# Optimization experiments

Measured on AMD Instinct MI355X. Metric: run time of the kernel, lower is better.

Reference implementation:

```python
import jax, jax.numpy as jnp
import numpy as np

C = 512
NUM_GROUPS = 32
EPS = 1e-6


def group_norm(x, gamma, beta):
    # x: [B, C, H, W]
    B, Cc, H, W = x.shape
    xg = x.reshape(B, NUM_GROUPS, Cc // NUM_GROUPS, H, W)
    mean = xg.mean(axis=(2, 3, 4), keepdims=True)
    var = xg.var(axis=(2, 3, 4), keepdims=True)
    xn = (xg - mean) / jnp.sqrt(var + EPS)
    xn = xn.reshape(B, Cc, H, W)
    return xn * gamma[None, :, None, None] + beta[None, :, None, None]


def conv1x1(x, w, b):
    # w: [out_c, in_c], x: [B, C, H, W]
    return jnp.einsum('oc,bchw->bohw', w, x) + b[None, :, None, None]


def setup_inputs() -> dict:
    key = jax.random.key(0)
    ks = jax.random.split(key, 6)
    B, H, W = 2, 64, 64
    x = jax.random.normal(ks[0], (B, C, H, W), dtype=jnp.float32)
    s = 1.0 / np.sqrt(C)
    wq = jax.random.normal(ks[1], (C, C), dtype=jnp.float32) * s
    wk = jax.random.normal(ks[2], (C, C), dtype=jnp.float32) * s
    wv = jax.random.normal(ks[3], (C, C), dtype=jnp.float32) * s
    wo = jax.random.normal(ks[4], (C, C), dtype=jnp.float32) * s
    bq = jnp.zeros((C,), jnp.float32)
    bk = jnp.zeros((C,), jnp.float32)
    bv = jnp.zeros((C,), jnp.float32)
    bo = jnp.zeros((C,), jnp.float32)
    gamma = jnp.ones((C,), jnp.float32)
    beta = jnp.zeros((C,), jnp.float32)
    return {"x": x, "gamma": gamma, "beta": beta, "wq": wq, "bq": bq,
            "wk": wk, "bk": bk, "wv": wv, "bv": bv, "wo": wo, "bo": bo}


def reference(x, gamma, beta, wq, bq, wk, bk, wv, bv, wo, bo):
    B, Cc, H, W = x.shape
    h = group_norm(x, gamma, beta)
    q = conv1x1(h, wq, bq).reshape(B, Cc, H * W)  # [B, C, N]
    k = conv1x1(h, wk, bk).reshape(B, Cc, H * W)
    v = conv1x1(h, wv, bv).reshape(B, Cc, H * W)
    scale = Cc ** (-0.5)
    # scores a[b,i,j] = sum_c q[b,c,i] * k[b,c,j]
    a = jnp.einsum('bci,bcj->bij', q, k) * scale
    a = jax.nn.softmax(a, axis=2)
    # out[b,c,i] = sum_j v[b,c,j] * a[b,i,j]  (matches bmm(v, a^T))
    o = jnp.einsum('bcj,bij->bci', v, a).reshape(B, Cc, H, W)
    o = conv1x1(o, wo, bo)
    return x + o
```

## Files before the change

kernel.cpp:

```cpp
#include <hip/hip_runtime.h>
#include <stdint.h>

#define NPIX 4096
#define CDIM 512

typedef _Float16 hv8 __attribute__((ext_vector_type(8)));
typedef float f32x4 __attribute__((ext_vector_type(4)));

__device__ __forceinline__ void lds_direct16(const _Float16* g, _Float16* l) {
    __builtin_amdgcn_global_load_lds(
        (const __attribute__((address_space(1))) void*)g,
        (__attribute__((address_space(3))) void*)l, 16, 0, 0);
}

__global__ void cvt_w(const float* __restrict__ s0, const float* __restrict__ s1,
                      const float* __restrict__ s2, const float* __restrict__ s3,
                      _Float16* __restrict__ d0, _Float16* __restrict__ d1,
                      _Float16* __restrict__ d2, _Float16* __restrict__ d3) {
    int i = blockIdx.x * 256 + threadIdx.x;
    d0[i] = (_Float16)s0[i];
    d1[i] = (_Float16)s1[i];
    d2[i] = (_Float16)s2[i];
    d3[i] = (_Float16)s3[i];
}

__global__ void stats_kernel(const float* __restrict__ x, float* __restrict__ stats) {
    int idx = blockIdx.x;
    const float4* base = (const float4*)(x + (long)idx * 16 * NPIX);
    int tid = threadIdx.x;
    float s = 0.f, sq = 0.f;
    for (int it = 0; it < 64; ++it) {
        float4 f = base[it * 256 + tid];
        s  += f.x + f.y + f.z + f.w;
        sq += f.x * f.x + f.y * f.y + f.z * f.z + f.w * f.w;
    }
    __shared__ float rs[256], rq[256];
    rs[tid] = s; rq[tid] = sq;
    __syncthreads();
    for (int st = 128; st > 0; st >>= 1) {
        if (tid < st) { rs[tid] += rs[tid + st]; rq[tid] += rq[tid + st]; }
        __syncthreads();
    }
    if (tid == 0) {
        float mean = rs[0] * (1.0f / 65536.0f);
        float var  = rq[0] * (1.0f / 65536.0f) - mean * mean;
        stats[idx * 2]     = mean;
        stats[idx * 2 + 1] = rsqrtf(var + 1e-6f);
    }
}

__global__ void normT_kernel(const float* __restrict__ x, const float* __restrict__ stats,
                             const float* __restrict__ gamma, const float* __restrict__ beta,
                             _Float16* __restrict__ hT) {
    int b = blockIdx.z, c0 = blockIdx.x * 32, n0 = blockIdx.y * 32;
    int tid = threadIdx.x;
    __shared__ float t[32][33];
    int cl = tid >> 5;
    int nl = tid & 31;
    for (int r = 0; r < 4; ++r)
        t[r * 8 + cl][nl] = x[(long)b * CDIM * NPIX + (long)(c0 + r * 8 + cl) * NPIX + n0 + nl];
    __syncthreads();
    for (int r = 0; r < 4; ++r) {
        int nr = r * 8 + cl;
        int c = c0 + nl;
        float m    = stats[(b * 32 + (c >> 4)) * 2];
        float rstd = stats[(b * 32 + (c >> 4)) * 2 + 1];
        float val = (t[nl][nr] - m) * rstd * gamma[c] + beta[c];
        hT[(long)b * NPIX * CDIM + (long)(n0 + nr) * CDIM + c] = (_Float16)val;
    }
}

template<int EPI>
__launch_bounds__(256, 2)
__global__ void gemm_bt_kernel(const _Float16* __restrict__ A, const _Float16* __restrict__ BT,
                               void* __restrict__ D, const float* __restrict__ bias,
                               const float* __restrict__ resid,
                               int M, int N, int K,
                               long aBatch, long bBatch, long dBatch, long rBatch) {
    const int b = blockIdx.z;
    A  += (long)b * aBatch;
    BT += (long)b * bBatch;
    const int m0 = blockIdx.y * 128;
    const int n0 = blockIdx.x * 128;
    const int tid = threadIdx.x;
    const int l = tid & 63;
    const int w = tid >> 6;
    const int wm = (w >> 1) * 64;
    const int wn = (w & 1) * 64;
    const int lr = l & 15;
    const int lk = l >> 4;
    __shared__ __align__(16) _Float16 As[128 * 32];
    __shared__ __align__(16) _Float16 Bs[128 * 32];
    f32x4 acc[4][4] = {};
    const int nK = K >> 5;
    for (int kt = 0; kt < nK; ++kt) {
        const int kb = kt * 32;
#pragma unroll
        for (int c = 0; c < 2; ++c) {
            int chunk = c * 256 + tid;
            int row = chunk >> 2;
            int k8 = (chunk & 3) * 8;
            _Float16* ldsA = As + (size_t)(c * 256 + (tid & ~63)) * 8;
            _Float16* ldsB = Bs + (size_t)(c * 256 + (tid & ~63)) * 8;
            lds_direct16(A  + (long)(m0 + row) * K + kb + k8, ldsA);
            lds_direct16(BT + (long)(n0 + row) * K + kb + k8, ldsB);
        }
        __syncthreads();
        hv8 af[4], bfr[4];
#pragma unroll
        for (int mi = 0; mi < 4; ++mi)
            af[mi] = *(const hv8*)(As + (size_t)(wm + mi * 16 + lr) * 32 + lk * 8);
#pragma unroll
        for (int ni = 0; ni < 4; ++ni)
            bfr[ni] = *(const hv8*)(Bs + (size_t)(wn + ni * 16 + lr) * 32 + lk * 8);
#pragma unroll
        for (int mi = 0; mi < 4; ++mi)
#pragma unroll
            for (int ni = 0; ni < 4; ++ni)
                acc[mi][ni] = __builtin_amdgcn_mfma_f32_16x16x32_f16(af[mi], bfr[ni], acc[mi][ni], 0, 0, 0);
        __syncthreads();
    }
#pragma unroll
    for (int mi = 0; mi < 4; ++mi)
#pragma unroll
        for (int ni = 0; ni < 4; ++ni)
#pragma unroll
            for (int r = 0; r < 4; ++r) {
                int row = m0 + wm + mi * 16 + lk * 4 + r;
                int col = n0 + wn + ni * 16 + lr;
                float val = acc[mi][ni][r];
                if (EPI == 0) {
                    ((_Float16*)D)[(long)b * dBatch + (long)row * N + col] = (_Float16)(val + bias[col]);
                } else if (EPI == 1) {
                    ((_Float16*)D)[(long)b * dBatch + (long)row * N + col] = (_Float16)(val + bias[row]);
                } else {
                    long idx = (long)row * N + col;
                    ((float*)D)[(long)b * dBatch + idx] =
                        val + bias[row] + resid[(long)b * rBatch + idx];
                }
            }
}

__launch_bounds__(512, 2)
__global__ void attn_kernel(const _Float16* __restrict__ qT, const _Float16* __restrict__ kT,
                            const _Float16* __restrict__ v,
                            _Float16* __restrict__ p0, _Float16* __restrict__ p1,
                            float* __restrict__ lbuf) {
    __shared__ __align__(16) _Float16 Ks[2][32 * 512];
    __shared__ __align__(16) char ps[2][64 * 80];
    __shared__ float red[8][64];
    __shared__ float redt[64];

    const int g = blockIdx.x;
    const int xcd = g & 7;
    const int comb = xcd >> 1;
    const int itile = ((g >> 3) << 1) | (xcd & 1);
    const int batch = comb >> 1;
    const int jhalf = comb & 1;
    const int i0 = itile * 64;
    const int jbase = jhalf * 2048;

    const int tid = threadIdx.x;
    const int l = tid & 63, w = tid >> 6;
    const int lr = l & 15, lk = l >> 4;
    const int iq = w >> 1, jq = w & 1;

    const _Float16* qb = qT + (long)batch * NPIX * CDIM;
    const _Float16* kb = kT + (long)batch * NPIX * CDIM;
    const _Float16* vb = v  + (long)batch * CDIM * NPIX;

    hv8 af[16];
    {
        const _Float16* qr = qb + (long)(i0 + iq * 16 + lr) * CDIM + lk * 8;
#pragma unroll
        for (int kk = 0; kk < 16; ++kk)
            af[kk] = *(const hv8*)(qr + kk * 32);
    }

    f32x4 oacc[4][4] = {};
    float lsum[4] = {};
    hv8 vf[4];

    const _Float16* vptr = vb + (long)(w * 64 + lr) * NPIX + jbase + lk * 8;
    const float scale = 0.044194173824159216f;

#define STAGE(BUF, JT)                                                               \
    {                                                                                \
        const long j0s = (long)jbase + (JT) * 32;                                    \
        _Float16* kd = Ks[BUF];                                                      \
        _Pragma("unroll")                                                            \
        for (int q = 0; q < 4; ++q) {                                                \
            int row = q * 8 + w;                                                     \
            int cc = l ^ (row & 7);                                                  \
            lds_direct16(kb + (j0s + row) * CDIM + cc * 8, kd + row * 512);          \
        }                                                                            \
    }

#define VLOAD(JT)                                                                    \
    {                                                                                \
        _Pragma("unroll")                                                            \
        for (int ni = 0; ni < 4; ++ni)                                               \
            vf[ni] = *(const hv8*)(vptr + (long)ni * (16 * NPIX) + (JT) * 32);       \
    }

#define QKEXP(CUR)                                                                   \
    {                                                                                \
        const char* kbase = (const char*)Ks[CUR];                                    \
        f32x4 sa = {}, sb = {};                                                      \
        const int jj = jq * 16 + lr;                                                 \
        const uint32_t sw = (uint32_t)((jj & 7) << 4);                               \
        _Pragma("unroll")                                                            \
        for (int kk = 0; kk < 8; ++kk) {                                             \
            hv8 b0 = *(const hv8*)(kbase + (((uint32_t)(jj * 1024 + (2 * kk) * 64 + lk * 16)) ^ sw));     \
            sa = __builtin_amdgcn_mfma_f32_16x16x32_f16(af[2 * kk], b0, sa, 0, 0, 0);                     \
            hv8 b1 = *(const hv8*)(kbase + (((uint32_t)(jj * 1024 + (2 * kk + 1) * 64 + lk * 16)) ^ sw)); \
            sb = __builtin_amdgcn_mfma_f32_16x16x32_f16(af[2 * kk + 1], b1, sb, 0, 0, 0);                 \
        }                                                                            \
        sa += sb;                                                                    \
        _Pragma("unroll")                                                            \
        for (int r = 0; r < 4; ++r) {                                                \
            float p = __expf(sa[r] * scale);                                         \
            lsum[r] += p;                                                            \
            int i = iq * 16 + lk * 4 + r;                                            \
            int j2 = jq * 16 + lr;                                                   \
            *(_Float16*)(ps[CUR] + i * 80 + j2 * 2) = (_Float16)p;                   \
        }                                                                            \
    }

#define PVSTEP(PRV)                                                                  \
    {                                                                                \
        _Pragma("unroll")                                                            \
        for (int mi = 0; mi < 4; ++mi) {                                             \
            int i2 = mi * 16 + lr;                                                   \
            hv8 pa = *(const hv8*)(ps[PRV] + i2 * 80 + lk * 16);                     \
            _Pragma("unroll")                                                        \
            for (int ni = 0; ni < 4; ++ni)                                           \
                oacc[mi][ni] = __builtin_amdgcn_mfma_f32_16x16x32_f16(pa, vf[ni], oacc[mi][ni], 0, 0, 0); \
        }                                                                            \
    }

#define ENDBAR(N)                                                                    \
    __builtin_amdgcn_sched_barrier(0);                                               \
    asm volatile("s_waitcnt vmcnt(" #N ") lgkmcnt(0)" ::: "memory");                 \
    __builtin_amdgcn_s_barrier();                                                    \
    __builtin_amdgcn_sched_barrier(0);

#define STEP(JT, CUR)                                                                \
    {                                                                                \
        if ((JT) < 63) STAGE((CUR) ^ 1, (JT) + 1)                                    \
        __builtin_amdgcn_sched_barrier(0);                                           \
        __builtin_amdgcn_s_setprio(1);                                               \
        QKEXP(CUR)                                                                   \
        PVSTEP((CUR) ^ 1)                                                            \
        __builtin_amdgcn_s_setprio(0);                                               \
        __builtin_amdgcn_sched_barrier(0);                                           \
        VLOAD(JT)                                                                    \
        ENDBAR(4)                                                                    \
    }

    STAGE(0, 0)
    __builtin_amdgcn_sched_barrier(0);
    asm volatile("s_waitcnt vmcnt(0)" ::: "memory");
    __builtin_amdgcn_s_barrier();
    __builtin_amdgcn_sched_barrier(0);

    STAGE(1, 1)
    __builtin_amdgcn_s_setprio(1);
    QKEXP(0)
    __builtin_amdgcn_s_setprio(0);
    VLOAD(0)
    ENDBAR(4)

    for (int jt = 1; jt < 63; jt += 2) {
        STEP(jt,     1)
        STEP(jt + 1, 0)
    }
    STEP(63, 1)

    asm volatile("s_waitcnt vmcnt(0)" ::: "memory");
    __builtin_amdgcn_sched_barrier(0);
    PVSTEP(1)

#pragma unroll
    for (int m = 1; m <= 8; m <<= 1)
#pragma unroll
        for (int r = 0; r < 4; ++r)
            lsum[r] += __shfl_xor(lsum[r], m, 64);
    if (lr == 0)
#pragma unroll
        for (int r = 0; r < 4; ++r)
            red[w][iq * 16 + lk * 4 + r] = lsum[r];
    __syncthreads();
    if (tid < 64) {
        int iq2 = tid >> 4;
        float lv = red[iq2 * 2][tid] + red[iq2 * 2 + 1][tid];
        redt[tid] = 1.0f / lv;
        lbuf[jhalf * 8192 + batch * NPIX + i0 + tid] = lv;
    }
    __syncthreads();

    _Float16* dsth = (jhalf ? p1 : p0) + (long)batch * NPIX * CDIM;
#pragma unroll
    for (int mi = 0; mi < 4; ++mi)
#pragma unroll
        for (int r = 0; r < 4; ++r) {
            int row = mi * 16 + lk * 4 + r;
            float rv = redt[row];
#pragma unroll
            for (int ni = 0; ni < 4; ++ni) {
                int c = w * 64 + ni * 16 + lr;
                dsth[(long)(i0 + row) * CDIM + c] = (_Float16)(oacc[mi][ni][r] * rv);
            }
        }
#undef STEP
#undef ENDBAR
#undef PVSTEP
#undef QKEXP
#undef VLOAD
#undef STAGE
}

__global__ void combine_kernel(const _Float16* __restrict__ p0, const _Float16* __restrict__ p1,
                               const float* __restrict__ lbuf, _Float16* __restrict__ out) {
    long g = (long)blockIdx.x * 256 + threadIdx.x;
    long base = g * 8;
    int rowg = (int)(g >> 6);
    float l0 = lbuf[rowg], l1 = lbuf[8192 + rowg];
    float w0 = l0 / (l0 + l1);
    float w1 = 1.0f - w0;
    hv8 a = *(const hv8*)(p0 + base);
    hv8 b = *(const hv8*)(p1 + base);
    hv8 o;
#pragma unroll
    for (int i = 0; i < 8; ++i)
        o[i] = (_Float16)((float)a[i] * w0 + (float)b[i] * w1);
    *(hv8*)(out + base) = o;
}

extern "C" void kernel_launch(void* const* d_in, const int* in_sizes, int n_in,
                              void* d_out, int out_size, void* d_ws, size_t ws_size,
                              hipStream_t stream) {
    const float* x     = (const float*)d_in[0];
    const float* gamma = (const float*)d_in[1];
    const float* beta  = (const float*)d_in[2];
    const float* wq    = (const float*)d_in[3];
    const float* bq    = (const float*)d_in[4];
    const float* wk    = (const float*)d_in[5];
    const float* bk    = (const float*)d_in[6];
    const float* wv    = (const float*)d_in[7];
    const float* bv    = (const float*)d_in[8];
    const float* wo    = (const float*)d_in[9];
    const float* bo    = (const float*)d_in[10];
    float* out = (float*)d_out;

    char* ws = (char*)d_ws;
    float* stats = (float*)ws;
    _Float16* wqb = (_Float16*)(ws + 1024);
    _Float16* wkb = wqb + 262144;
    _Float16* wvb = wkb + 262144;
    _Float16* wob = wvb + 262144;
    _Float16* hT  = wob + 262144;
    const long TSZ = (long)2 * NPIX * CDIM;
    _Float16* qT = hT + TSZ;
    _Float16* kT = qT + TSZ;
    _Float16* vv = kT + TSZ;
    _Float16* oT = vv + TSZ;
    float* lbuf = (float*)(oT + TSZ);

    cvt_w<<<dim3(1024), dim3(256), 0, stream>>>(wq, wk, wv, wo, wqb, wkb, wvb, wob);
    stats_kernel<<<dim3(64), dim3(256), 0, stream>>>(x, stats);
    normT_kernel<<<dim3(16, 128, 2), dim3(256), 0, stream>>>(x, stats, gamma, beta, hT);

    const long NC = (long)NPIX * CDIM;
    gemm_bt_kernel<0><<<dim3(4, 32, 2), dim3(256), 0, stream>>>(
        hT, wqb, (void*)qT, bq, nullptr, NPIX, CDIM, CDIM, NC, 0L, NC, 0L);
    gemm_bt_kernel<0><<<dim3(4, 32, 2), dim3(256), 0, stream>>>(
        hT, wkb, (void*)kT, bk, nullptr, NPIX, CDIM, CDIM, NC, 0L, NC, 0L);
    gemm_bt_kernel<1><<<dim3(32, 4, 2), dim3(256), 0, stream>>>(
        wvb, hT, (void*)vv, bv, nullptr, CDIM, NPIX, CDIM, 0L, NC, NC, 0L);

    attn_kernel<<<dim3(256), dim3(512), 0, stream>>>(qT, kT, vv, oT, hT, lbuf);

    combine_kernel<<<dim3(2048), dim3(256), 0, stream>>>(oT, hT, lbuf, qT);

    gemm_bt_kernel<2><<<dim3(32, 4, 2), dim3(256), 0, stream>>>(
        wob, qT, (void*)out, bo, x, CDIM, NPIX, CDIM, 0L, NC, NC, NC);
}
```

Before: 191.9 us.

## Double key tile to 64 per step and reuse each K fragment across two query rows

The attention kernel now stages 64 keys per pipeline step instead of 32, which halves the number of barrier-separated iterations. The wave layout changes from 4x2 to 2x4 over (query, key), so each wave computes two 16-row query subtiles against one 16-key slice and every K fragment read from LDS feeds two MFMAs. Q fragments in registers double (af[2][16]), and LDS for K and the probability buffer grows to about 146 KB. This may cut occupancy below the two blocks per CU requested by launch bounds, and raises register pressure.

```diff
diff --git a/kernel.cpp b/kernel.cpp
--- a/kernel.cpp
+++ b/kernel.cpp
@@ -146,8 +146,8 @@
                             const _Float16* __restrict__ v,
                             _Float16* __restrict__ p0, _Float16* __restrict__ p1,
                             float* __restrict__ lbuf) {
-    __shared__ __align__(16) _Float16 Ks[2][32 * 512];
-    __shared__ __align__(16) char ps[2][64 * 80];
+    __shared__ __align__(16) _Float16 Ks[2][64 * 512];
+    __shared__ __align__(16) char ps[2][64 * 144];
     __shared__ float red[8][64];
     __shared__ float redt[64];
 
@@ -163,33 +163,34 @@
     const int tid = threadIdx.x;
     const int l = tid & 63, w = tid >> 6;
     const int lr = l & 15, lk = l >> 4;
-    const int iq = w >> 1, jq = w & 1;
+    const int iq = w >> 2, jq = w & 3;
 
     const _Float16* qb = qT + (long)batch * NPIX * CDIM;
     const _Float16* kb = kT + (long)batch * NPIX * CDIM;
     const _Float16* vb = v  + (long)batch * CDIM * NPIX;
 
-    hv8 af[16];
-    {
-        const _Float16* qr = qb + (long)(i0 + iq * 16 + lr) * CDIM + lk * 8;
+    hv8 af[2][16];
+#pragma unroll
+    for (int s = 0; s < 2; ++s) {
+        const _Float16* qr = qb + (long)(i0 + iq * 32 + s * 16 + lr) * CDIM + lk * 8;
 #pragma unroll
         for (int kk = 0; kk < 16; ++kk)
-            af[kk] = *(const hv8*)(qr + kk * 32);
+            af[s][kk] = *(const hv8*)(qr + kk * 32);
     }
 
     f32x4 oacc[4][4] = {};
-    float lsum[4] = {};
-    hv8 vf[4];
+    float lsum[2][4] = {};
+    hv8 vf[4][2];
 
     const _Float16* vptr = vb + (long)(w * 64 + lr) * NPIX + jbase + lk * 8;
     const float scale = 0.044194173824159216f;
 
 #define STAGE(BUF, JT)                                                               \
     {                                                                                \
-        const long j0s = (long)jbase + (JT) * 32;                                    \
+        const long j0s = (long)jbase + (JT) * 64;                                    \
         _Float16* kd = Ks[BUF];                                                      \
         _Pragma("unroll")                                                            \
-        for (int q = 0; q < 4; ++q) {                                                \
+        for (int q = 0; q < 8; ++q) {                                                \
             int row = q * 8 + w;                                                     \
             int cc = l ^ (row & 7);                                                  \
             lds_direct16(kb + (j0s + row) * CDIM + cc * 8, kd + row * 512);          \
@@ -200,30 +201,33 @@
     {                                                                                \
         _Pragma("unroll")                                                            \
         for (int ni = 0; ni < 4; ++ni)                                               \
-            vf[ni] = *(const hv8*)(vptr + (long)ni * (16 * NPIX) + (JT) * 32);       \
+            _Pragma("unroll")                                                        \
+            for (int jh = 0; jh < 2; ++jh)                                           \
+                vf[ni][jh] = *(const hv8*)(vptr + (long)ni * (16 * NPIX) + (JT) * 64 + jh * 32); \
     }
 
 #define QKEXP(CUR)                                                                   \
     {                                                                                \
         const char* kbase = (const char*)Ks[CUR];                                    \
-        f32x4 sa = {}, sb = {};                                                      \
+        f32x4 s0 = {}, s1 = {};                                                      \
         const int jj = jq * 16 + lr;                                                 \
         const uint32_t sw = (uint32_t)((jj & 7) << 4);                               \
         _Pragma("unroll")                                                            \
-        for (int kk = 0; kk < 8; ++kk) {                                             \
-            hv8 b0 = *(const hv8*)(kbase + (((uint32_t)(jj * 1024 + (2 * kk) * 64 + lk * 16)) ^ sw));     \
-            sa = __builtin_amdgcn_mfma_f32_16x16x32_f16(af[2 * kk], b0, sa, 0, 0, 0);                     \
-            hv8 b1 = *(const hv8*)(kbase + (((uint32_t)(jj * 1024 + (2 * kk + 1) * 64 + lk * 16)) ^ sw)); \
-            sb = __builtin_amdgcn_mfma_f32_16x16x32_f16(af[2 * kk + 1], b1, sb, 0, 0, 0);                 \
+        for (int kk = 0; kk < 16; ++kk) {                                            \
+            hv8 bf = *(const hv8*)(kbase + (((uint32_t)(jj * 1024 + kk * 64 + lk * 16)) ^ sw)); \
+            s0 = __builtin_amdgcn_mfma_f32_16x16x32_f16(af[0][kk], bf, s0, 0, 0, 0); \
+            s1 = __builtin_amdgcn_mfma_f32_16x16x32_f16(af[1][kk], bf, s1, 0, 0, 0); \
         }                                                                            \
-        sa += sb;                                                                    \
         _Pragma("unroll")                                                            \
         for (int r = 0; r < 4; ++r) {                                                \
-            float p = __expf(sa[r] * scale);                                         \
-            lsum[r] += p;                                                            \
-            int i = iq * 16 + lk * 4 + r;                                            \
+            float pe0 = __expf(s0[r] * scale);                                       \
+            float pe1 = __expf(s1[r] * scale);                                       \
+            lsum[0][r] += pe0;                                                       \
+            lsum[1][r] += pe1;                                                       \
+            int ia = iq * 32 + lk * 4 + r;                                           \
             int j2 = jq * 16 + lr;                                                   \
-            *(_Float16*)(ps[CUR] + i * 80 + j2 * 2) = (_Float16)p;                   \
+            *(_Float16*)(ps[CUR] + ia * 144 + j2 * 2) = (_Float16)pe0;               \
+            *(_Float16*)(ps[CUR] + (ia + 16) * 144 + j2 * 2) = (_Float16)pe1;        \
         }                                                                            \
     }
 
@@ -231,11 +235,14 @@
     {                                                                                \
         _Pragma("unroll")                                                            \
         for (int mi = 0; mi < 4; ++mi) {                                             \
-            int i2 = mi * 16 + lr;                                                   \
-            hv8 pa = *(const hv8*)(ps[PRV] + i2 * 80 + lk * 16);                     \
+            int row = mi * 16 + lr;                                                  \
             _Pragma("unroll")                                                        \
-            for (int ni = 0; ni < 4; ++ni)                                           \
-                oacc[mi][ni] = __builtin_amdgcn_mfma_f32_16x16x32_f16(pa, vf[ni], oacc[mi][ni], 0, 0, 0); \
+            for (int jh = 0; jh < 2; ++jh) {                                         \
+                hv8 pa = *(const hv8*)(ps[PRV] + row * 144 + jh * 64 + lk * 16);     \
+                _Pragma("unroll")                                                    \
+                for (int ni = 0; ni < 4; ++ni)                                       \
+                    oacc[mi][ni] = __builtin_amdgcn_mfma_f32_16x16x32_f16(pa, vf[ni][jh], oacc[mi][ni], 0, 0, 0); \
+            }                                                                        \
         }                                                                            \
     }
 
@@ -247,7 +254,7 @@
 
 #define STEP(JT, CUR)                                                                \
     {                                                                                \
-        if ((JT) < 63) STAGE((CUR) ^ 1, (JT) + 1)                                    \
+        if ((JT) < 31) STAGE((CUR) ^ 1, (JT) + 1)                                    \
         __builtin_amdgcn_sched_barrier(0);                                           \
         __builtin_amdgcn_s_setprio(1);                                               \
         QKEXP(CUR)                                                                   \
@@ -255,7 +262,7 @@
         __builtin_amdgcn_s_setprio(0);                                               \
         __builtin_amdgcn_sched_barrier(0);                                           \
         VLOAD(JT)                                                                    \
-        ENDBAR(4)                                                                    \
+        ENDBAR(8)                                                                    \
     }
 
     STAGE(0, 0)
@@ -269,13 +276,13 @@
     QKEXP(0)
     __builtin_amdgcn_s_setprio(0);
     VLOAD(0)
-    ENDBAR(4)
-
-    for (int jt = 1; jt < 63; jt += 2) {
+    ENDBAR(8)
+
+    for (int jt = 1; jt < 31; jt += 2) {
         STEP(jt,     1)
         STEP(jt + 1, 0)
     }
-    STEP(63, 1)
+    STEP(31, 1)
 
     asm volatile("s_waitcnt vmcnt(0)" ::: "memory");
     __builtin_amdgcn_sched_barrier(0);
@@ -284,16 +291,21 @@
 #pragma unroll
     for (int m = 1; m <= 8; m <<= 1)
 #pragma unroll
-        for (int r = 0; r < 4; ++r)
-            lsum[r] += __shfl_xor(lsum[r], m, 64);
+        for (int s = 0; s < 2; ++s)
+#pragma unroll
+            for (int r = 0; r < 4; ++r)
+                lsum[s][r] += __shfl_xor(lsum[s][r], m, 64);
     if (lr == 0)
 #pragma unroll
-        for (int r = 0; r < 4; ++r)
-            red[w][iq * 16 + lk * 4 + r] = lsum[r];
+        for (int s = 0; s < 2; ++s)
+#pragma unroll
+            for (int r = 0; r < 4; ++r)
+                red[w][iq * 32 + s * 16 + lk * 4 + r] = lsum[s][r];
     __syncthreads();
     if (tid < 64) {
-        int iq2 = tid >> 4;
-        float lv = red[iq2 * 2][tid] + red[iq2 * 2 + 1][tid];
+        int iq2 = tid >> 5;
+        float lv = red[iq2 * 4 + 0][tid] + red[iq2 * 4 + 1][tid]
+                 + red[iq2 * 4 + 2][tid] + red[iq2 * 4 + 3][tid];
         redt[tid] = 1.0f / lv;
         lbuf[jhalf * 8192 + batch * NPIX + i0 + tid] = lv;
     }
```

New measurement: 426.0 us. 2.22x slower.

## Split group-norm stats across more blocks and fuse Q/K projections into one GEMM

Applied to the files above, without the earlier changes.

The group statistics pass now runs 512 blocks, each producing partial sums over one eighth of a group. The normalize kernel reduces the eight partials itself, which removes a low-occupancy 64-block reduction. The Q and K projections become a single GEMM with N=1024 against the contiguous wq/wk half-precision buffers and a concatenated bias, and a new epilogue routes columns to the qT or kT buffers. This saves one kernel launch and a second read of hT, at the cost of redundant partial-sum reads in every normalize block.

```diff
diff --git a/kernel.cpp b/kernel.cpp
--- a/kernel.cpp
+++ b/kernel.cpp
@@ -16,20 +16,26 @@
 __global__ void cvt_w(const float* __restrict__ s0, const float* __restrict__ s1,
                       const float* __restrict__ s2, const float* __restrict__ s3,
                       _Float16* __restrict__ d0, _Float16* __restrict__ d1,
-                      _Float16* __restrict__ d2, _Float16* __restrict__ d3) {
+                      _Float16* __restrict__ d2, _Float16* __restrict__ d3,
+                      const float* __restrict__ bq, const float* __restrict__ bk,
+                      float* __restrict__ bqk) {
     int i = blockIdx.x * 256 + threadIdx.x;
     d0[i] = (_Float16)s0[i];
     d1[i] = (_Float16)s1[i];
     d2[i] = (_Float16)s2[i];
     d3[i] = (_Float16)s3[i];
-}
-
-__global__ void stats_kernel(const float* __restrict__ x, float* __restrict__ stats) {
-    int idx = blockIdx.x;
-    const float4* base = (const float4*)(x + (long)idx * 16 * NPIX);
+    if (i < 512) { bqk[i] = bq[i]; bqk[i + 512] = bk[i]; }
+}
+
+__global__ void pstats_kernel(const float* __restrict__ x,
+                              float* __restrict__ partS, float* __restrict__ partQ) {
+    int pb = blockIdx.x;
+    int gi = pb >> 3;
+    int sl = pb & 7;
+    const float4* base = (const float4*)x + (long)gi * 16384 + sl * 2048;
     int tid = threadIdx.x;
     float s = 0.f, sq = 0.f;
-    for (int it = 0; it < 64; ++it) {
+    for (int it = 0; it < 8; ++it) {
         float4 f = base[it * 256 + tid];
         s  += f.x + f.y + f.z + f.w;
         sq += f.x * f.x + f.y * f.y + f.z * f.z + f.w * f.w;
@@ -41,15 +47,11 @@
         if (tid < st) { rs[tid] += rs[tid + st]; rq[tid] += rq[tid + st]; }
         __syncthreads();
     }
-    if (tid == 0) {
-        float mean = rs[0] * (1.0f / 65536.0f);
-        float var  = rq[0] * (1.0f / 65536.0f) - mean * mean;
-        stats[idx * 2]     = mean;
-        stats[idx * 2 + 1] = rsqrtf(var + 1e-6f);
-    }
-}
-
-__global__ void normT_kernel(const float* __restrict__ x, const float* __restrict__ stats,
+    if (tid == 0) { partS[pb] = rs[0]; partQ[pb] = rq[0]; }
+}
+
+__global__ void normT_kernel(const float* __restrict__ x,
+                             const float* __restrict__ partS, const float* __restrict__ partQ,
                              const float* __restrict__ gamma, const float* __restrict__ beta,
                              _Float16* __restrict__ hT) {
     int b = blockIdx.z, c0 = blockIdx.x * 32, n0 = blockIdx.y * 32;
@@ -60,12 +62,17 @@
     for (int r = 0; r < 4; ++r)
         t[r * 8 + cl][nl] = x[(long)b * CDIM * NPIX + (long)(c0 + r * 8 + cl) * NPIX + n0 + nl];
     __syncthreads();
+    int c = c0 + nl;
+    int gg = b * 32 + (c >> 4);
+    float s = 0.f, q = 0.f;
+#pragma unroll
+    for (int k2 = 0; k2 < 8; ++k2) { s += partS[gg * 8 + k2]; q += partQ[gg * 8 + k2]; }
+    float m    = s * (1.0f / 65536.0f);
+    float rstd = rsqrtf(q * (1.0f / 65536.0f) - m * m + 1e-6f);
+    float gm = gamma[c], bt = beta[c];
     for (int r = 0; r < 4; ++r) {
         int nr = r * 8 + cl;
-        int c = c0 + nl;
-        float m    = stats[(b * 32 + (c >> 4)) * 2];
-        float rstd = stats[(b * 32 + (c >> 4)) * 2 + 1];
-        float val = (t[nl][nr] - m) * rstd * gamma[c] + beta[c];
+        float val = (t[nl][nr] - m) * rstd * gm + bt;
         hT[(long)b * NPIX * CDIM + (long)(n0 + nr) * CDIM + c] = (_Float16)val;
     }
 }
@@ -133,10 +140,14 @@
                     ((_Float16*)D)[(long)b * dBatch + (long)row * N + col] = (_Float16)(val + bias[col]);
                 } else if (EPI == 1) {
                     ((_Float16*)D)[(long)b * dBatch + (long)row * N + col] = (_Float16)(val + bias[row]);
-                } else {
+                } else if (EPI == 2) {
                     long idx = (long)row * N + col;
                     ((float*)D)[(long)b * dBatch + idx] =
                         val + bias[row] + resid[(long)b * rBatch + idx];
+                } else {
+                    long qoff = (long)(col >> 9) * (2L * NPIX * CDIM);
+                    ((_Float16*)D)[qoff + (long)b * dBatch + (long)row * CDIM + (col & 511)] =
+                        (_Float16)(val + bias[col]);
                 }
             }
 }
@@ -354,8 +365,10 @@
     float* out = (float*)d_out;
 
     char* ws = (char*)d_ws;
-    float* stats = (float*)ws;
-    _Float16* wqb = (_Float16*)(ws + 1024);
+    float* partS = (float*)ws;
+    float* partQ = partS + 512;
+    float* bqk   = partQ + 512;
+    _Float16* wqb = (_Float16*)(ws + 8192);
     _Float16* wkb = wqb + 262144;
     _Float16* wvb = wkb + 262144;
     _Float16* wob = wvb + 262144;
@@ -367,15 +380,14 @@
     _Float16* oT = vv + TSZ;
     float* lbuf = (float*)(oT + TSZ);
 
-    cvt_w<<<dim3(1024), dim3(256), 0, stream>>>(wq, wk, wv, wo, wqb, wkb, wvb, wob);
-    stats_kernel<<<dim3(64), dim3(256), 0, stream>>>(x, stats);
-    normT_kernel<<<dim3(16, 128, 2), dim3(256), 0, stream>>>(x, stats, gamma, beta, hT);
+    cvt_w<<<dim3(1024), dim3(256), 0, stream>>>(wq, wk, wv, wo, wqb, wkb, wvb, wob,
+                                                bq, bk, bqk);
+    pstats_kernel<<<dim3(512), dim3(256), 0, stream>>>(x, partS, partQ);
+    normT_kernel<<<dim3(16, 128, 2), dim3(256), 0, stream>>>(x, partS, partQ, gamma, beta, hT);
 
     const long NC = (long)NPIX * CDIM;
-    gemm_bt_kernel<0><<<dim3(4, 32, 2), dim3(256), 0, stream>>>(
-        hT, wqb, (void*)qT, bq, nullptr, NPIX, CDIM, CDIM, NC, 0L, NC, 0L);
-    gemm_bt_kernel<0><<<dim3(4, 32, 2), dim3(256), 0, stream>>>(
-        hT, wkb, (void*)kT, bk, nullptr, NPIX, CDIM, CDIM, NC, 0L, NC, 0L);
+    gemm_bt_kernel<3><<<dim3(8, 32, 2), dim3(256), 0, stream>>>(
+        hT, wqb, (void*)qT, bqk, nullptr, NPIX, 1024, CDIM, NC, 0L, NC, 0L);
     gemm_bt_kernel<1><<<dim3(32, 4, 2), dim3(256), 0, stream>>>(
         wvb, hT, (void*)vv, bv, nullptr, CDIM, NPIX, CDIM, 0L, NC, NC, 0L);
 
```

Result: faster. 181.5 us (-5.4%).
